# Kernel tuning notes

Measured on AMD Instinct MI355X. Metric: run time of the kernel, lower is better.

Reference implementation:

```python
import jax, jax.numpy as jnp
import numpy as np
import math


def setup_inputs() -> dict:
    key = jax.random.key(0)
    kq, kk, kv = jax.random.split(key, 3)
    B, HQ, HKV, S, D = 1, 32, 8, 2048, 128
    query = jax.random.normal(kq, (B, HQ, S, D), dtype=jnp.float32)
    key_s = jax.random.normal(kk, (B, HKV, S, D), dtype=jnp.float32)
    value = jax.random.normal(kv, (B, HKV, S, D), dtype=jnp.float32)
    # additive causal mask [B,1,S,S]: 0 where j<=i, large-negative elsewhere
    neg = jnp.finfo(jnp.float32).min
    i = jnp.arange(S)
    attention_mask = jnp.where(i[None, :] <= i[:, None], 0.0, neg).astype(jnp.float32)[None, None]
    return {"query": query, "key": key_s, "value": value,
            "attention_mask": attention_mask, "window_size": 1024}


def reference(query, key, value, attention_mask, window_size):
    B, HQ, S, D = query.shape
    groups = HQ // key.shape[1]
    scaling = 1.0 / math.sqrt(D)
    # repeat_kv (GQA -> MHA)
    k = jnp.repeat(key, groups, axis=1)   # [B,HQ,S,D]
    v = jnp.repeat(value, groups, axis=1)
    # ---- eager_attention_forward ----
    scores = jnp.einsum('bhqd,bhkd->bhqk', query, k) * scaling
    scores = scores + attention_mask[:, :, :, :S]
    attn_weights = jax.nn.softmax(scores.astype(jnp.float32), axis=-1).astype(query.dtype)
    attn_output = jnp.einsum('bhqk,bhkd->bhqd', attn_weights, v)
    attn_output = attn_output.transpose(0, 2, 1, 3)  # [B,S,HQ,D]
    # ---- compute_window_attn_weights ----
    W = window_size
    qw = query[:, :, -W:, :]                                  # [B,HQ,W,D]
    ww = jnp.einsum('bhqd,bhkd->bhqk', qw, k) / math.sqrt(D)  # [B,HQ,W,S]
    neg = jnp.finfo(ww.dtype).min
    r = jnp.arange(W)
    win_mask = jnp.where(r[None, :] <= r[:, None], 0.0, neg).astype(ww.dtype)  # [W,W]
    ww = ww.at[:, :, :, -W:].add(win_mask[None, None])
    window_attn_weights = jax.nn.softmax(ww.astype(jnp.float32), axis=-1).astype(query.dtype)
    return (attn_output, attn_weights, window_attn_weights)
```

## Files before the change

kernel.cpp:

```cpp
#include <hip/hip_runtime.h>
#include <hip/hip_bf16.h>

typedef __bf16 bf16x8 __attribute__((ext_vector_type(8)));
typedef float f32x4 __attribute__((ext_vector_type(4)));
static_assert(sizeof(bf16x8) == 16, "bf16x8 must be 16B");

constexpr int S = 2048, D = 128, HQ = 32, W = 1024;
constexpr float SCALE_L2E = 0.08838834764831845f * 1.4426950408889634f;

constexpr size_t O1 = (size_t)S * HQ * D;
constexpr size_t O2 = O1 + (size_t)HQ * S * S;
constexpr int TILE_BYTES = 64 * 256;

__device__ __forceinline__ void gl_lds16(const void* g, void* l) {
    __builtin_amdgcn_global_load_lds(
        (const __attribute__((address_space(1))) void*)(unsigned long long)g,
        (__attribute__((address_space(3))) void*)(unsigned int)(unsigned long long)l,
        16, 0, 0);
}
__device__ __forceinline__ void st4(float* p, f32x4 v) {
    *reinterpret_cast<f32x4*>(p) = v;
}

__global__ __launch_bounds__(256)
void prep_kernel(const float* __restrict__ K, const float* __restrict__ V,
                 char* __restrict__ KbI, char* __restrict__ VtI)
{
    __shared__ __attribute__((aligned(16))) __bf16 Vs[128][72];
    const int b = blockIdx.x, hkv = b >> 5, kt = b & 31;
    const int tid = threadIdx.x;
    const float* Ks   = K + ((size_t)hkv * S + kt * 64) * D;
    const float* Vsrc = V + ((size_t)hkv * S + kt * 64) * D;
    char* Kimg = KbI + (size_t)(hkv * 32 + kt) * TILE_BYTES;
    char* Vimg = VtI + (size_t)(hkv * 32 + kt) * TILE_BYTES;

    #pragma unroll
    for (int i = 0; i < 4; ++i) {
        int idx = tid + i * 256;
        int r = idx >> 4, sl = idx & 15;
        float4 a = *reinterpret_cast<const float4*>(Ks + r * D + sl * 8);
        float4 c = *reinterpret_cast<const float4*>(Ks + r * D + sl * 8 + 4);
        bf16x8 f = {(__bf16)a.x, (__bf16)a.y, (__bf16)a.z, (__bf16)a.w,
                    (__bf16)c.x, (__bf16)c.y, (__bf16)c.z, (__bf16)c.w};
        *reinterpret_cast<bf16x8*>(Kimg + r * 256 + ((sl * 16) ^ ((r & 7) << 4))) = f;
    }
    #pragma unroll
    for (int i = 0; i < 8; ++i) {
        int idx = tid + i * 256;
        int r = idx >> 5, c = (idx & 31) * 4;
        float4 vv = *reinterpret_cast<const float4*>(Vsrc + r * D + c);
        Vs[c + 0][r] = (__bf16)vv.x; Vs[c + 1][r] = (__bf16)vv.y;
        Vs[c + 2][r] = (__bf16)vv.z; Vs[c + 3][r] = (__bf16)vv.w;
    }
    __syncthreads();
    #pragma unroll
    for (int i = 0; i < 4; ++i) {
        int idx = tid + i * 256;
        int d = idx >> 3, sl = idx & 7;
        bf16x8 v = *reinterpret_cast<const bf16x8*>(&Vs[d][sl * 8]);
        *reinterpret_cast<bf16x8*>(Vimg + d * 128 + ((sl * 16) ^ ((d & 7) << 4))) = v;
    }
}

__global__ __launch_bounds__(256, 4)
void attn_fused4(const float* __restrict__ Q, const char* __restrict__ KbI,
                 const char* __restrict__ VtI, float* __restrict__ out)
{
    __shared__ __attribute__((aligned(16))) char LDS_K[TILE_BYTES];
    __shared__ __attribute__((aligned(16))) char LDS_V[TILE_BYTES];
    __shared__ __attribute__((aligned(16))) char LDS_P[4][2048];

    const int bid = blockIdx.x;
    const int j   = bid >> 5;
    const int qt = (j < 8) ? (16 + j) : (j < 16) ? (23 - j) : (j < 24) ? (47 - j) : (j - 24);
    const int b5 = bid & 31;
    const int h  = (b5 & 7) * 4 + (b5 >> 3);
    const int hkv = h >> 2;
    const int q0  = qt << 6;
    const int tid = threadIdx.x, wave = tid >> 6, lane = tid & 63;
    const int lo = lane & 15, hi = lane >> 4;
    const int qw0 = q0 + wave * 16;
    const bool winw = (qt >= 16);

    const char* Ktiles = KbI + (size_t)hkv * 32 * TILE_BYTES;
    const char* Vtiles = VtI + (size_t)hkv * 32 * TILE_BYTES;
    const float* Qh = Q + (size_t)h * S * D;

    bf16x8 qf[4];
    {
        const float* qs = Qh + (size_t)(qw0 + lo) * D + hi * 8;
        #pragma unroll
        for (int dc = 0; dc < 4; ++dc) {
            float4 a = *reinterpret_cast<const float4*>(qs + dc * 32);
            float4 b = *reinterpret_cast<const float4*>(qs + dc * 32 + 4);
            bf16x8 f;
            f[0] = (__bf16)(a.x * SCALE_L2E); f[1] = (__bf16)(a.y * SCALE_L2E);
            f[2] = (__bf16)(a.z * SCALE_L2E); f[3] = (__bf16)(a.w * SCALE_L2E);
            f[4] = (__bf16)(b.x * SCALE_L2E); f[5] = (__bf16)(b.y * SCALE_L2E);
            f[6] = (__bf16)(b.z * SCALE_L2E); f[7] = (__bf16)(b.w * SCALE_L2E);
            qf[dc] = f;
        }
    }

    float lsum[4] = {0.f, 0.f, 0.f, 0.f};
    for (int kt = 0; kt <= qt; ++kt) {
        const char* src = Ktiles + (size_t)kt * TILE_BYTES;
        #pragma unroll
        for (int i = 0; i < 4; ++i)
            gl_lds16(src + (wave * 4 + i) * 1024 + lane * 16,
                     LDS_K + (wave * 4 + i) * 1024);
        __builtin_amdgcn_sched_barrier(0);
        asm volatile("s_waitcnt vmcnt(0)" ::: "memory");
        __builtin_amdgcn_s_barrier();
        __builtin_amdgcn_sched_barrier(0);
        #pragma unroll
        for (int cg = 0; cg < 4; ++cg) {
            f32x4 acc = {0.f, 0.f, 0.f, 0.f};
            const int row = cg * 16 + lo, swzr = (row & 7) << 4;
            #pragma unroll
            for (int dc = 0; dc < 4; ++dc) {
                bf16x8 kf = *reinterpret_cast<const bf16x8*>(
                    LDS_K + row * 256 + ((hi * 16 + dc * 64) ^ swzr));
                acc = __builtin_amdgcn_mfma_f32_16x16x32_bf16(qf[dc], kf, acc, 0, 0, 0);
            }
            const int k = (kt << 6) + cg * 16 + lo;
            #pragma unroll
            for (int r = 0; r < 4; ++r) {
                int q = qw0 + hi * 4 + r;
                lsum[r] += (k <= q) ? exp2f(acc[r]) : 0.f;
            }
        }
        __builtin_amdgcn_sched_barrier(0);
        asm volatile("s_waitcnt lgkmcnt(0)" ::: "memory");
        __builtin_amdgcn_s_barrier();
        __builtin_amdgcn_sched_barrier(0);
    }
    float rcp_[4];
    #pragma unroll
    for (int r = 0; r < 4; ++r) {
        float v = lsum[r];
        v += __shfl_xor(v, 1); v += __shfl_xor(v, 2);
        v += __shfl_xor(v, 4); v += __shfl_xor(v, 8);
        rcp_[r] = 1.0f / v;
    }

    f32x4 oacc[8];
    #pragma unroll
    for (int i = 0; i < 8; ++i) oacc[i] = (f32x4){0.f, 0.f, 0.f, 0.f};
    char* Ps = LDS_P[wave];

    for (int kt = 0; kt <= qt; ++kt) {
        const char* sk = Ktiles + (size_t)kt * TILE_BYTES;
        const char* sv = Vtiles + (size_t)kt * TILE_BYTES;
        #pragma unroll
        for (int i = 0; i < 4; ++i) {
            gl_lds16(sk + (wave * 4 + i) * 1024 + lane * 16, LDS_K + (wave * 4 + i) * 1024);
            gl_lds16(sv + (wave * 4 + i) * 1024 + lane * 16, LDS_V + (wave * 4 + i) * 1024);
        }
        __builtin_amdgcn_sched_barrier(0);
        asm volatile("s_waitcnt vmcnt(0)" ::: "memory");
        __builtin_amdgcn_s_barrier();
        __builtin_amdgcn_sched_barrier(0);

        const int kbase = kt << 6;

        #pragma unroll
        for (int cg = 0; cg < 4; ++cg) {
            f32x4 acc = {0.f, 0.f, 0.f, 0.f};
            const int row = cg * 16 + lo, swzr = (row & 7) << 4;
            #pragma unroll
            for (int dc = 0; dc < 4; ++dc) {
                bf16x8 kf = *reinterpret_cast<const bf16x8*>(
                    LDS_K + row * 256 + ((hi * 16 + dc * 64) ^ swzr));
                acc = __builtin_amdgcn_mfma_f32_16x16x32_bf16(qf[dc], kf, acc, 0, 0, 0);
            }
            const int k = kbase + cg * 16 + lo;
            #pragma unroll
            for (int r = 0; r < 4; ++r) {
                const int q = qw0 + hi * 4 + r;
                float pv = (k <= q) ? exp2f(acc[r]) * rcp_[r] : 0.f;
                const int prow = hi * 4 + r;
                *reinterpret_cast<__bf16*>(
                    Ps + prow * 128 + ((2 * (cg * 16 + lo)) ^ ((prow & 7) << 4))) = (__bf16)pv;
            }
        }

        {
            const int row = lane >> 2;
            const int q = qw0 + row;
            float* dstP = out + O1 + ((size_t)h * S + q) * S + kbase;
            #pragma unroll
            for (int t = 0; t < 2; ++t) {
                int boff = (((lane & 3) * 16 + t * 64) ^ ((row & 7) << 4));
                bf16x8 pv8 = *reinterpret_cast<const bf16x8*>(Ps + row * 128 + boff);
                f32x4 f0 = {(float)pv8[0], (float)pv8[1], (float)pv8[2], (float)pv8[3]};
                f32x4 f1 = {(float)pv8[4], (float)pv8[5], (float)pv8[6], (float)pv8[7]};
                int k0 = (lane & 3) * 8 + t * 32;
                st4(dstP + k0, f0);
                st4(dstP + k0 + 4, f1);
                if (winw) {
                    float* dstW = out + O2 + ((size_t)h * W + (q - W)) * S + kbase;
                    st4(dstW + k0, f0);
                    st4(dstW + k0 + 4, f1);
                }
            }
        }

        #pragma unroll
        for (int kc = 0; kc < 2; ++kc) {
            const int cb = (kc * 64 + hi * 16) ^ ((lo & 7) << 4);
            bf16x8 pf = *reinterpret_cast<const bf16x8*>(Ps + lo * 128 + cb);
            #pragma unroll
            for (int dg = 0; dg < 8; ++dg) {
                bf16x8 vf = *reinterpret_cast<const bf16x8*>(LDS_V + (dg * 16 + lo) * 128 + cb);
                oacc[dg] = __builtin_amdgcn_mfma_f32_16x16x32_bf16(pf, vf, oacc[dg], 0, 0, 0);
            }
        }

        __builtin_amdgcn_sched_barrier(0);
        asm volatile("s_waitcnt lgkmcnt(0)" ::: "memory");
        __builtin_amdgcn_s_barrier();
        __builtin_amdgcn_sched_barrier(0);
    }

    {
        const int zr = lane >> 2;
        const int c0 = (lane & 3) * 16;
        const f32x4 z = {0.f, 0.f, 0.f, 0.f};
        const int q = qw0 + zr;
        for (int kt = qt + 1; kt < 32; ++kt) {
            float* dp = out + O1 + ((size_t)h * S + q) * S + kt * 64 + c0;
            #pragma unroll
            for (int jj = 0; jj < 4; ++jj) st4(dp + jj * 4, z);
            if (winw) {
                float* dw = out + O2 + ((size_t)h * W + (q - W)) * S + kt * 64 + c0;
                #pragma unroll
                for (int jj = 0; jj < 4; ++jj) st4(dw + jj * 4, z);
            }
        }
    }

    #pragma unroll
    for (int dg = 0; dg < 8; ++dg) {
        #pragma unroll
        for (int r = 0; r < 4; ++r) {
            const int q = qw0 + hi * 4 + r;
            out[((size_t)q * HQ + h) * D + dg * 16 + lo] = oacc[dg][r];
        }
    }
}

extern "C" void kernel_launch(void* const* d_in, const int* in_sizes, int n_in,
                              void* d_out, int out_size, void* d_ws, size_t ws_size,
                              hipStream_t stream)
{
    const float* Q = (const float*)d_in[0];
    const float* K = (const float*)d_in[1];
    const float* V = (const float*)d_in[2];
    float* out = (float*)d_out;

    char* KbI = (char*)d_ws;
    char* VtI = (char*)d_ws + (size_t)4 * 1024 * 1024;

    hipLaunchKernelGGL(prep_kernel, dim3(256),  dim3(256), 0, stream, K, V, KbI, VtI);
    hipLaunchKernelGGL(attn_fused4, dim3(1024), dim3(256), 0, stream, Q, KbI, VtI, out);
}
```

Measured before the change: 300.6 us.

## Double-buffer K/V tiles in LDS and halve the PV-pass tile size

Both the row-sum pass and the output pass now prefetch the next K (and V) tile into a second LDS buffer while the current tile is being computed. The second pass moves to 32-key tiles, and the prep kernel re-lays out the transposed V image into 32-column sub-images to match. The per-iteration barrier wait uses partial vmcnt counts so the outstanding probability stores do not block the next tile's loads. The goal is to hide global-to-LDS load latency behind MFMA work and the large attention-weight stores. The cost is twice as many loop iterations and barriers in the PV pass, and the wait counts depend on the exact number of stores issued per iteration.

```diff
diff --git a/kernel.cpp b/kernel.cpp
--- a/kernel.cpp
+++ b/kernel.cpp
@@ -10,7 +10,8 @@
 
 constexpr size_t O1 = (size_t)S * HQ * D;
 constexpr size_t O2 = O1 + (size_t)HQ * S * S;
-constexpr int TILE_BYTES = 64 * 256;
+constexpr int TILE64 = 64 * 256;
+constexpr int TILE32 = 32 * 256;
 
 __device__ __forceinline__ void gl_lds16(const void* g, void* l) {
     __builtin_amdgcn_global_load_lds(
@@ -31,8 +32,8 @@
     const int tid = threadIdx.x;
     const float* Ks   = K + ((size_t)hkv * S + kt * 64) * D;
     const float* Vsrc = V + ((size_t)hkv * S + kt * 64) * D;
-    char* Kimg = KbI + (size_t)(hkv * 32 + kt) * TILE_BYTES;
-    char* Vimg = VtI + (size_t)(hkv * 32 + kt) * TILE_BYTES;
+    char* Kimg = KbI + (size_t)(hkv * 32 + kt) * TILE64;
+    char* Vimg = VtI + (size_t)(hkv * 32 + kt) * TILE64;
 
     #pragma unroll
     for (int i = 0; i < 4; ++i) {
@@ -56,19 +57,20 @@
     #pragma unroll
     for (int i = 0; i < 4; ++i) {
         int idx = tid + i * 256;
-        int d = idx >> 3, sl = idx & 7;
-        bf16x8 v = *reinterpret_cast<const bf16x8*>(&Vs[d][sl * 8]);
-        *reinterpret_cast<bf16x8*>(Vimg + d * 128 + ((sl * 16) ^ ((d & 7) << 4))) = v;
+        int img = idx >> 9;
+        int rem = idx & 511;
+        int d = rem >> 2, sl = rem & 3;
+        bf16x8 v = *reinterpret_cast<const bf16x8*>(&Vs[d][img * 32 + sl * 8]);
+        *reinterpret_cast<bf16x8*>(Vimg + img * TILE32 + d * 64 + ((sl * 16) ^ ((d & 3) << 4))) = v;
     }
 }
 
 __global__ __launch_bounds__(256, 4)
-void attn_fused4(const float* __restrict__ Q, const char* __restrict__ KbI,
+void attn_fused5(const float* __restrict__ Q, const char* __restrict__ KbI,
                  const char* __restrict__ VtI, float* __restrict__ out)
 {
-    __shared__ __attribute__((aligned(16))) char LDS_K[TILE_BYTES];
-    __shared__ __attribute__((aligned(16))) char LDS_V[TILE_BYTES];
-    __shared__ __attribute__((aligned(16))) char LDS_P[4][2048];
+    __shared__ __attribute__((aligned(16))) char BUF[4][TILE32];
+    __shared__ __attribute__((aligned(16))) char PST[4][1024];
 
     const int bid = blockIdx.x;
     const int j   = bid >> 5;
@@ -82,8 +84,8 @@
     const int qw0 = q0 + wave * 16;
     const bool winw = (qt >= 16);
 
-    const char* Ktiles = KbI + (size_t)hkv * 32 * TILE_BYTES;
-    const char* Vtiles = VtI + (size_t)hkv * 32 * TILE_BYTES;
+    const char* Ktiles = KbI + (size_t)hkv * 32 * TILE64;
+    const char* Vtiles = VtI + (size_t)hkv * 32 * TILE64;
     const float* Qh = Q + (size_t)h * S * D;
 
     bf16x8 qf[4];
@@ -103,37 +105,50 @@
     }
 
     float lsum[4] = {0.f, 0.f, 0.f, 0.f};
-    for (int kt = 0; kt <= qt; ++kt) {
-        const char* src = Ktiles + (size_t)kt * TILE_BYTES;
+    {
         #pragma unroll
         for (int i = 0; i < 4; ++i)
-            gl_lds16(src + (wave * 4 + i) * 1024 + lane * 16,
-                     LDS_K + (wave * 4 + i) * 1024);
+            gl_lds16(Ktiles + (wave * 4 + i) * 1024 + lane * 16,
+                     &BUF[0][0] + (wave * 4 + i) * 1024);
         __builtin_amdgcn_sched_barrier(0);
         asm volatile("s_waitcnt vmcnt(0)" ::: "memory");
         __builtin_amdgcn_s_barrier();
         __builtin_amdgcn_sched_barrier(0);
-        #pragma unroll
-        for (int cg = 0; cg < 4; ++cg) {
-            f32x4 acc = {0.f, 0.f, 0.f, 0.f};
-            const int row = cg * 16 + lo, swzr = (row & 7) << 4;
-            #pragma unroll
-            for (int dc = 0; dc < 4; ++dc) {
-                bf16x8 kf = *reinterpret_cast<const bf16x8*>(
-                    LDS_K + row * 256 + ((hi * 16 + dc * 64) ^ swzr));
-                acc = __builtin_amdgcn_mfma_f32_16x16x32_bf16(qf[dc], kf, acc, 0, 0, 0);
-            }
-            const int k = (kt << 6) + cg * 16 + lo;
-            #pragma unroll
-            for (int r = 0; r < 4; ++r) {
-                int q = qw0 + hi * 4 + r;
-                lsum[r] += (k <= q) ? exp2f(acc[r]) : 0.f;
-            }
-        }
-        __builtin_amdgcn_sched_barrier(0);
-        asm volatile("s_waitcnt lgkmcnt(0)" ::: "memory");
-        __builtin_amdgcn_s_barrier();
-        __builtin_amdgcn_sched_barrier(0);
+
+        int cur = 0;
+        for (int kt = 0; kt <= qt; ++kt) {
+            if (kt < qt) {
+                const char* src = Ktiles + (size_t)(kt + 1) * TILE64;
+                char* dst = &BUF[(cur ^ 1) * 2][0];
+                #pragma unroll
+                for (int i = 0; i < 4; ++i)
+                    gl_lds16(src + (wave * 4 + i) * 1024 + lane * 16, dst + (wave * 4 + i) * 1024);
+                __builtin_amdgcn_sched_barrier(0);
+            }
+            const char* KtB = &BUF[cur * 2][0];
+            #pragma unroll
+            for (int cg = 0; cg < 4; ++cg) {
+                f32x4 acc = {0.f, 0.f, 0.f, 0.f};
+                const int row = cg * 16 + lo, swzr = (row & 7) << 4;
+                #pragma unroll
+                for (int dc = 0; dc < 4; ++dc) {
+                    bf16x8 kf = *reinterpret_cast<const bf16x8*>(
+                        KtB + row * 256 + ((hi * 16 + dc * 64) ^ swzr));
+                    acc = __builtin_amdgcn_mfma_f32_16x16x32_bf16(qf[dc], kf, acc, 0, 0, 0);
+                }
+                const int k = (kt << 6) + cg * 16 + lo;
+                #pragma unroll
+                for (int r = 0; r < 4; ++r) {
+                    int q = qw0 + hi * 4 + r;
+                    lsum[r] += (k <= q) ? exp2f(acc[r]) : 0.f;
+                }
+            }
+            __builtin_amdgcn_sched_barrier(0);
+            asm volatile("s_waitcnt vmcnt(0) lgkmcnt(0)" ::: "memory");
+            __builtin_amdgcn_s_barrier();
+            __builtin_amdgcn_sched_barrier(0);
+            cur ^= 1;
+        }
     }
     float rcp_[4];
     #pragma unroll
@@ -147,31 +162,48 @@
     f32x4 oacc[8];
     #pragma unroll
     for (int i = 0; i < 8; ++i) oacc[i] = (f32x4){0.f, 0.f, 0.f, 0.f};
-    char* Ps = LDS_P[wave];
-
-    for (int kt = 0; kt <= qt; ++kt) {
-        const char* sk = Ktiles + (size_t)kt * TILE_BYTES;
-        const char* sv = Vtiles + (size_t)kt * TILE_BYTES;
-        #pragma unroll
-        for (int i = 0; i < 4; ++i) {
-            gl_lds16(sk + (wave * 4 + i) * 1024 + lane * 16, LDS_K + (wave * 4 + i) * 1024);
-            gl_lds16(sv + (wave * 4 + i) * 1024 + lane * 16, LDS_V + (wave * 4 + i) * 1024);
+    char* Ps = PST[wave];
+    const int nk32 = (qt + 1) * 2;
+
+    {
+        #pragma unroll
+        for (int i = 0; i < 2; ++i) {
+            gl_lds16(Ktiles + (wave * 2 + i) * 1024 + lane * 16, &BUF[0][0] + (wave * 2 + i) * 1024);
+            gl_lds16(Vtiles + (wave * 2 + i) * 1024 + lane * 16, &BUF[2][0] + (wave * 2 + i) * 1024);
         }
         __builtin_amdgcn_sched_barrier(0);
         asm volatile("s_waitcnt vmcnt(0)" ::: "memory");
         __builtin_amdgcn_s_barrier();
         __builtin_amdgcn_sched_barrier(0);
-
-        const int kbase = kt << 6;
-
-        #pragma unroll
-        for (int cg = 0; cg < 4; ++cg) {
+    }
+
+    int cur = 0;
+    for (int t = 0; t < nk32; ++t) {
+        const bool more = (t + 1 < nk32);
+        if (more) {
+            const char* sk = Ktiles + (size_t)(t + 1) * TILE32;
+            const char* sv = Vtiles + (size_t)(t + 1) * TILE32;
+            char* dk = &BUF[cur ^ 1][0];
+            char* dv = &BUF[2 + (cur ^ 1)][0];
+            #pragma unroll
+            for (int i = 0; i < 2; ++i) {
+                gl_lds16(sk + (wave * 2 + i) * 1024 + lane * 16, dk + (wave * 2 + i) * 1024);
+                gl_lds16(sv + (wave * 2 + i) * 1024 + lane * 16, dv + (wave * 2 + i) * 1024);
+            }
+            __builtin_amdgcn_sched_barrier(0);
+        }
+        const char* KtB = &BUF[cur][0];
+        const char* VtB = &BUF[2 + cur][0];
+        const int kbase = t * 32;
+
+        #pragma unroll
+        for (int cg = 0; cg < 2; ++cg) {
             f32x4 acc = {0.f, 0.f, 0.f, 0.f};
             const int row = cg * 16 + lo, swzr = (row & 7) << 4;
             #pragma unroll
             for (int dc = 0; dc < 4; ++dc) {
                 bf16x8 kf = *reinterpret_cast<const bf16x8*>(
-                    LDS_K + row * 256 + ((hi * 16 + dc * 64) ^ swzr));
+                    KtB + row * 256 + ((hi * 16 + dc * 64) ^ swzr));
                 acc = __builtin_amdgcn_mfma_f32_16x16x32_bf16(qf[dc], kf, acc, 0, 0, 0);
             }
             const int k = kbase + cg * 16 + lo;
@@ -181,46 +213,48 @@
                 float pv = (k <= q) ? exp2f(acc[r]) * rcp_[r] : 0.f;
                 const int prow = hi * 4 + r;
                 *reinterpret_cast<__bf16*>(
-                    Ps + prow * 128 + ((2 * (cg * 16 + lo)) ^ ((prow & 7) << 4))) = (__bf16)pv;
+                    Ps + prow * 64 + ((2 * (cg * 16 + lo)) ^ ((prow & 3) << 4))) = (__bf16)pv;
             }
         }
 
         {
             const int row = lane >> 2;
+            const int sl  = lane & 3;
             const int q = qw0 + row;
-            float* dstP = out + O1 + ((size_t)h * S + q) * S + kbase;
-            #pragma unroll
-            for (int t = 0; t < 2; ++t) {
-                int boff = (((lane & 3) * 16 + t * 64) ^ ((row & 7) << 4));
-                bf16x8 pv8 = *reinterpret_cast<const bf16x8*>(Ps + row * 128 + boff);
-                f32x4 f0 = {(float)pv8[0], (float)pv8[1], (float)pv8[2], (float)pv8[3]};
-                f32x4 f1 = {(float)pv8[4], (float)pv8[5], (float)pv8[6], (float)pv8[7]};
-                int k0 = (lane & 3) * 8 + t * 32;
-                st4(dstP + k0, f0);
-                st4(dstP + k0 + 4, f1);
-                if (winw) {
-                    float* dstW = out + O2 + ((size_t)h * W + (q - W)) * S + kbase;
-                    st4(dstW + k0, f0);
-                    st4(dstW + k0 + 4, f1);
-                }
-            }
-        }
-
-        #pragma unroll
-        for (int kc = 0; kc < 2; ++kc) {
-            const int cb = (kc * 64 + hi * 16) ^ ((lo & 7) << 4);
-            bf16x8 pf = *reinterpret_cast<const bf16x8*>(Ps + lo * 128 + cb);
+            bf16x8 pv8 = *reinterpret_cast<const bf16x8*>(
+                Ps + row * 64 + ((sl * 16) ^ ((row & 3) << 4)));
+            f32x4 f0 = {(float)pv8[0], (float)pv8[1], (float)pv8[2], (float)pv8[3]};
+            f32x4 f1 = {(float)pv8[4], (float)pv8[5], (float)pv8[6], (float)pv8[7]};
+            float* dstP = out + O1 + ((size_t)h * S + q) * S + kbase + sl * 8;
+            st4(dstP, f0);
+            st4(dstP + 4, f1);
+            if (winw) {
+                float* dstW = out + O2 + ((size_t)h * W + (q - W)) * S + kbase + sl * 8;
+                st4(dstW, f0);
+                st4(dstW + 4, f1);
+            }
+        }
+
+        {
+            bf16x8 pf = *reinterpret_cast<const bf16x8*>(
+                Ps + lo * 64 + ((hi * 16) ^ ((lo & 3) << 4)));
             #pragma unroll
             for (int dg = 0; dg < 8; ++dg) {
-                bf16x8 vf = *reinterpret_cast<const bf16x8*>(LDS_V + (dg * 16 + lo) * 128 + cb);
+                const int d = dg * 16 + lo;
+                bf16x8 vf = *reinterpret_cast<const bf16x8*>(
+                    VtB + d * 64 + ((hi * 16) ^ ((d & 3) << 4)));
                 oacc[dg] = __builtin_amdgcn_mfma_f32_16x16x32_bf16(pf, vf, oacc[dg], 0, 0, 0);
             }
         }
 
-        __builtin_amdgcn_sched_barrier(0);
-        asm volatile("s_waitcnt lgkmcnt(0)" ::: "memory");
-        __builtin_amdgcn_s_barrier();
-        __builtin_amdgcn_sched_barrier(0);
+        if (more) {
+            __builtin_amdgcn_sched_barrier(0);
+            if (winw) asm volatile("s_waitcnt vmcnt(4) lgkmcnt(0)" ::: "memory");
+            else      asm volatile("s_waitcnt vmcnt(2) lgkmcnt(0)" ::: "memory");
+            __builtin_amdgcn_s_barrier();
+            __builtin_amdgcn_sched_barrier(0);
+        }
+        cur ^= 1;
     }
 
     {
@@ -263,5 +297,5 @@
     char* VtI = (char*)d_ws + (size_t)4 * 1024 * 1024;
 
     hipLaunchKernelGGL(prep_kernel, dim3(256),  dim3(256), 0, stream, K, V, KbI, VtI);
-    hipLaunchKernelGGL(attn_fused4, dim3(1024), dim3(256), 0, stream, Q, KbI, VtI, out);
-}
+    hipLaunchKernelGGL(attn_fused5, dim3(1024), dim3(256), 0, stream, Q, KbI, VtI, out);
+}
```

After: 277.0 us. -7.9%, faster.
